# Kernel optimization log

Hardware: AMD Instinct MI355X
Metric: run time of the kernel (lower is better)

Reference implementation:

```python
import jax, jax.numpy as jnp
import numpy as np

V, H, B, S, J, T, NOP = 30000, 512, 16, 256, 10, 8, 4
NEG = -1e9


def setup_inputs() -> dict:
    key = jax.random.key(0)
    ks = jax.random.split(key, 10)
    return {
        "x": jax.random.randint(ks[0], (B, S), 0, V),
        "encoder_output": jax.random.normal(ks[1], (B, S, H), jnp.float32),
        "encoder_hidden": jax.random.normal(ks[2], (B, H), jnp.float32),
        "max_len": T,
        "emb_W": jax.random.normal(ks[3], (V, H), jnp.float32) * 0.02,
        "slot_emb": jax.random.normal(ks[4], (J, H), jnp.float32) * 0.1,
        "W_ih": jax.random.normal(ks[5], (3 * H, H), jnp.float32) * 0.02,
        "W_hh": jax.random.normal(ks[6], (3 * H, H), jnp.float32) * 0.02,
        "b_ih": jnp.zeros((3 * H,), jnp.float32),
        "b_hh": jnp.zeros((3 * H,), jnp.float32),
        "w_gen_W": jax.random.normal(ks[7], (1, 3 * H), jnp.float32) * 0.02,
        "w_gen_b": jnp.zeros((1,), jnp.float32),
        "action_W": jax.random.normal(ks[8], (NOP, H), jnp.float32) * 0.02,
        "action_b": jnp.zeros((NOP,), jnp.float32),
    }


def gru_step(xin, h, W_ih, W_hh, b_ih, b_hh):
    # xin, h: (J, B, H). PyTorch GRU gate order: r, z, n.
    gi = xin @ W_ih.T + b_ih
    gh = h @ W_hh.T + b_hh
    ir, iz, inn = jnp.split(gi, 3, axis=-1)
    hr, hz, hn = jnp.split(gh, 3, axis=-1)
    r = jax.nn.sigmoid(ir + hr)
    z = jax.nn.sigmoid(iz + hz)
    n = jnp.tanh(inn + r * hn)
    return (1.0 - z) * n + z * h


def reference(x, encoder_output, encoder_hidden, max_len, emb_W, slot_emb,
              W_ih, W_hh, b_ih, b_hh, w_gen_W, w_gen_b, action_W, action_b):
    nJ, nH = slot_emb.shape
    nB, nS = x.shape
    nV = emb_W.shape[0]
    mask = (x == 0)  # (B, S) pad mask
    xJ = jnp.broadcast_to(x[None], (nJ, nB, nS))
    jidx = jnp.arange(nJ)[:, None, None]
    bidx = jnp.arange(nB)[None, :, None]

    w0 = jnp.broadcast_to(slot_emb[:, None, :], (nJ, nB, nH))  # slot query per slot
    h0 = jnp.broadcast_to(encoder_hidden[None], (nJ, nB, nH))

    def step(carry, _):
        w, h = carry
        h = gru_step(w, h, W_ih, W_hh, b_ih, b_hh)
        # attention over encoder states
        attn_e = jnp.einsum('bsh,jbh->jbs', encoder_output, h)
        attn_e = jnp.where(mask[None], NEG, attn_e)
        attn_hist = jax.nn.softmax(attn_e, axis=-1)          # (J,B,S)
        context = jnp.einsum('jbs,bsh->jbh', attn_hist, encoder_output)
        # vocab distribution
        attn_vocab = jax.nn.softmax(h @ emb_W.T, axis=-1)    # (J,B,V)
        # pointer-generator mix
        gen_in = jnp.concatenate([w, h, context], axis=-1)   # (J,B,3H)
        p_gen = jax.nn.sigmoid(gen_in @ w_gen_W.T + w_gen_b) # (J,B,1)
        p_ctx = jnp.zeros((nJ, nB, nV), attn_vocab.dtype).at[jidx, bidx, xJ].add(attn_hist)
        p_final = p_gen * attn_vocab + (1.0 - p_gen) * p_ctx # (J,B,V)
        w_idx = jnp.argmax(p_final, axis=-1)                 # greedy next token
        w_next = emb_W[w_idx]                                # (J,B,H)
        return (w_next, h), (p_final, context)

    (_, _), (p_all, ctx_all) = jax.lax.scan(step, (w0, h0), None, length=max_len)
    # gate head uses context from first decode step (k == 0)
    gates = ctx_all[0] @ action_W.T + action_b               # (J,B,n_op)
    all_gate = jnp.transpose(gates, (1, 0, 2))               # (B,J,n_op)
    all_point = jnp.transpose(p_all, (2, 1, 0, 3))           # (B,J,T,V)
    return all_gate, all_point
```

## Files before the change

### kernel.cpp

```cpp
#include <hip/hip_runtime.h>
#include <math.h>

#define V 30000
#define H 512
#define NB 16
#define NS 256
#define NJ 10
#define NT 8
#define NOPS 4
#define NR 160
#define EV 30720
#define NEGV -1e9f
#define NTILES 1875
#define NVB 235

typedef __attribute__((ext_vector_type(8))) short short8;
typedef __attribute__((ext_vector_type(4))) short short4v;
typedef __attribute__((ext_vector_type(4))) float f32x4;

__device__ inline float bf2f(unsigned short s) {
    union { unsigned int u; float f; } c; c.u = ((unsigned int)s) << 16;
    return c.f;
}
__device__ inline unsigned short f2bf(float f) {
    union { float f; unsigned int u; } c; c.f = f;
    unsigned int u = c.u;
    u += 0x7fffu + ((u >> 16) & 1u);
    return (unsigned short)(u >> 16);
}
__device__ inline unsigned long long packkey(float f, int v) {
    union { float f; unsigned int u; } c; c.f = f;
    return ((unsigned long long)c.u << 32) | (unsigned int)(0x7FFFFFFF - v);
}

__global__ __launch_bounds__(256) void k_setup_pack(const float* __restrict__ emb,
                                                    unsigned short* __restrict__ emb_pk) {
    __shared__ unsigned short L[16 * 512];
    int nt = blockIdx.x;
    int t = threadIdx.x;
#pragma unroll
    for (int i = 0; i < 4; i++) {
        int o = i * 2048 + t * 8;
        int row = o >> 9, k = o & 511;
        const float4* src = (const float4*)(emb + (size_t)(nt * 16 + row) * 512 + k);
        float4 a = src[0], b = src[1];
        short8 v;
        v[0] = (short)f2bf(a.x); v[1] = (short)f2bf(a.y); v[2] = (short)f2bf(a.z); v[3] = (short)f2bf(a.w);
        v[4] = (short)f2bf(b.x); v[5] = (short)f2bf(b.y); v[6] = (short)f2bf(b.z); v[7] = (short)f2bf(b.w);
        *(short8*)(L + o) = v;
    }
    __syncthreads();
#pragma unroll
    for (int i = 0; i < 4; i++) {
        int idx = i * 256 + t;
        int ks = idx >> 6, l = idx & 63;
        int col15 = l & 15, quad = l >> 4;
        short8 v = *(const short8*)(L + col15 * 512 + ks * 32 + quad * 8);
        *(short8*)(emb_pk + ((size_t)(nt * 16 + ks) * 64 + l) * 8) = v;
    }
}

__global__ void k_setup_small(const float* __restrict__ Wih, const float* __restrict__ Whh,
    unsigned short* wih_hi, unsigned short* wih_lo, unsigned short* whh_hi, unsigned short* whh_lo,
    const float* __restrict__ slot, const float* __restrict__ ench,
    float* w_g, unsigned short* w_hi, unsigned short* w_lo,
    float* h_g, unsigned short* h_hi, unsigned short* h_lo, unsigned short* h_pk)
{
    int gid = blockIdx.x * 256 + threadIdx.x;
    if (gid < 786432) {
        float v1 = Wih[gid];
        unsigned short hi = f2bf(v1);
        wih_hi[gid] = hi; wih_lo[gid] = f2bf(v1 - bf2f(hi));
        float v2 = Whh[gid];
        hi = f2bf(v2);
        whh_hi[gid] = hi; whh_lo[gid] = f2bf(v2 - bf2f(hi));
    } else {
        int i = gid - 786432;
        if (i < NR * H) {
            int jb = i >> 9, d = i & 511;
            int j = jb >> 4, b = jb & 15;
            float wv = slot[j * H + d];
            w_g[i] = wv;
            unsigned short hi = f2bf(wv);
            w_hi[i] = hi; w_lo[i] = f2bf(wv - bf2f(hi));
            float hv = ench[b * H + d];
            h_g[i] = hv;
            hi = f2bf(hv);
            h_hi[i] = hi; h_lo[i] = f2bf(hv - bf2f(hi));
            int ks = d >> 5, quad = (d >> 3) & 3, e = d & 7;
            h_pk[(((jb >> 4) * 16 + ks) * 64 + quad * 16 + (jb & 15)) * 8 + e] = hi;
        }
    }
}

#define GRU_APAD 520
__global__ __launch_bounds__(256) void k_gru_gemm(
    const unsigned short* __restrict__ w_hi, const unsigned short* __restrict__ w_lo,
    const unsigned short* __restrict__ h_hi, const unsigned short* __restrict__ h_lo,
    const unsigned short* __restrict__ wih_hi, const unsigned short* __restrict__ wih_lo,
    const unsigned short* __restrict__ whh_hi, const unsigned short* __restrict__ whh_lo,
    float* __restrict__ gi, float* __restrict__ gh)
{
    __shared__ unsigned short Ah[16 * GRU_APAD];
    __shared__ unsigned short Al[16 * GRU_APAD];
    int nch = blockIdx.x, mt = blockIdx.y, z = blockIdx.z;
    const unsigned short* Asrc_hi = z ? h_hi : w_hi;
    const unsigned short* Asrc_lo = z ? h_lo : w_lo;
    const unsigned short* Bhi = z ? whh_hi : wih_hi;
    const unsigned short* Blo = z ? whh_lo : wih_lo;
    float* outp = z ? gh : gi;
    int t = threadIdx.x;
    for (int i = t; i < 2048; i += 256) {
        int matl = i >> 10;
        int row = (i >> 6) & 15;
        int seg = i & 63;
        const unsigned short* src = (matl ? Asrc_lo : Asrc_hi) + (mt * 16 + row) * 512 + seg * 8;
        unsigned short* dst = (matl ? Al : Ah) + row * GRU_APAD + seg * 8;
        *(short8*)dst = *(const short8*)src;
    }
    __syncthreads();
    int wv = t >> 6, lane = t & 63;
    int col15 = lane & 15, quad = lane >> 4;
    f32x4 acc0 = {0.f, 0.f, 0.f, 0.f}, acc1 = {0.f, 0.f, 0.f, 0.f};
    int c0 = nch * 128 + wv * 32 + col15;
    int c1 = c0 + 16;
    const unsigned short* bhp0 = Bhi + c0 * 512 + quad * 8;
    const unsigned short* bhp1 = Bhi + c1 * 512 + quad * 8;
    const unsigned short* blp0 = Blo + c0 * 512 + quad * 8;
    const unsigned short* blp1 = Blo + c1 * 512 + quad * 8;
    const unsigned short* ahp = Ah + col15 * GRU_APAD + quad * 8;
    const unsigned short* alp = Al + col15 * GRU_APAD + quad * 8;
#pragma unroll
    for (int ks = 0; ks < 16; ks++) {
        int ko = ks * 32;
        short8 bh0 = *(const short8*)(bhp0 + ko);
        short8 bh1 = *(const short8*)(bhp1 + ko);
        short8 bl0 = *(const short8*)(blp0 + ko);
        short8 bl1 = *(const short8*)(blp1 + ko);
        short8 ah = *(const short8*)(ahp + ko);
        short8 al = *(const short8*)(alp + ko);
        acc0 = __builtin_amdgcn_mfma_f32_16x16x32_bf16(ah, bh0, acc0, 0, 0, 0);
        acc1 = __builtin_amdgcn_mfma_f32_16x16x32_bf16(ah, bh1, acc1, 0, 0, 0);
        acc0 = __builtin_amdgcn_mfma_f32_16x16x32_bf16(ah, bl0, acc0, 0, 0, 0);
        acc1 = __builtin_amdgcn_mfma_f32_16x16x32_bf16(ah, bl1, acc1, 0, 0, 0);
        acc0 = __builtin_amdgcn_mfma_f32_16x16x32_bf16(al, bh0, acc0, 0, 0, 0);
        acc1 = __builtin_amdgcn_mfma_f32_16x16x32_bf16(al, bh1, acc1, 0, 0, 0);
    }
#pragma unroll
    for (int r = 0; r < 4; r++) {
        int row = mt * 16 + quad * 4 + r;
        outp[row * 1536 + c0] = acc0[r];
        outp[row * 1536 + c1] = acc1[r];
    }
}

__global__ __launch_bounds__(256) void k_attention(
    const float* __restrict__ gi, const float* __restrict__ gh,
    const float* __restrict__ b_ih, const float* __restrict__ b_hh,
    float* __restrict__ h_g, unsigned short* __restrict__ h_hi, unsigned short* __restrict__ h_lo,
    unsigned short* __restrict__ h_pk,
    const float* __restrict__ enc, const int* __restrict__ x,
    const float* __restrict__ w_g, const float* __restrict__ wgenW, const float* __restrict__ wgenb,
    float* __restrict__ attn_g, float* __restrict__ pgen_g,
    float* __restrict__ ctx0, int store_ctx)
{
    __shared__ float h_lds[512];
    __shared__ float sc[256];
    __shared__ float red[256];
    __shared__ float ctxp[4 * 512];
    int jb = blockIdx.x;
    int b = jb & 15;
    int t = threadIdx.x;
    int m_pk = jb >> 4, c_pk = jb & 15;
    for (int d = t; d < 512; d += 256) {
        int base = jb * 1536;
        float ir = gi[base + d]        + b_ih[d];
        float iz = gi[base + 512 + d]  + b_ih[512 + d];
        float in = gi[base + 1024 + d] + b_ih[1024 + d];
        float hr = gh[base + d]        + b_hh[d];
        float hz = gh[base + 512 + d]  + b_hh[512 + d];
        float hn = gh[base + 1024 + d] + b_hh[1024 + d];
        float hold = h_g[jb * 512 + d];
        float r = 1.f / (1.f + expf(-(ir + hr)));
        float z = 1.f / (1.f + expf(-(iz + hz)));
        float n = tanhf(in + r * hn);
        float hnew = (1.f - z) * n + z * hold;
        h_lds[d] = hnew;
        h_g[jb * 512 + d] = hnew;
        unsigned short hi = f2bf(hnew);
        h_hi[jb * 512 + d] = hi;
        h_lo[jb * 512 + d] = f2bf(hnew - bf2f(hi));
        int ks = d >> 5, quad = (d >> 3) & 3, e = d & 7;
        h_pk[((m_pk * 16 + ks) * 64 + quad * 16 + c_pk) * 8 + e] = hi;
    }
    __syncthreads();
    int wid = t >> 6, lane = t & 63;
    float hreg[8];
#pragma unroll
    for (int i = 0; i < 8; i++) hreg[i] = h_lds[lane * 8 + i];
    const float* encb = enc + (size_t)b * NS * H;
    for (int s = wid; s < NS; s += 4) {
        const float4* er = (const float4*)(encb + s * 512 + lane * 8);
        float4 e0 = er[0], e1 = er[1];
        float p = e0.x * hreg[0] + e0.y * hreg[1] + e0.z * hreg[2] + e0.w * hreg[3]
                + e1.x * hreg[4] + e1.y * hreg[5] + e1.z * hreg[6] + e1.w * hreg[7];
#pragma unroll
        for (int off = 32; off > 0; off >>= 1) p += __shfl_down(p, off);
        if (lane == 0) sc[s] = (x[b * NS + s] == 0) ? NEGV : p;
    }
    __syncthreads();
    red[t] = sc[t];
    __syncthreads();
    for (int sft = 128; sft > 0; sft >>= 1) { if (t < sft) red[t] = fmaxf(red[t], red[t + sft]); __syncthreads(); }
    float m = red[0];
    __syncthreads();
    float e = expf(sc[t] - m);
    red[t] = e;
    __syncthreads();
    for (int sft = 128; sft > 0; sft >>= 1) { if (t < sft) red[t] += red[t + sft]; __syncthreads(); }
    float inv = 1.f / red[0];
    float p_s = e * inv;
    sc[t] = p_s;
    attn_g[jb * NS + t] = p_s;
    __syncthreads();
    {
        float cp[8] = {0.f,0.f,0.f,0.f,0.f,0.f,0.f,0.f};
        const float* encw = encb + lane * 8;
        for (int s = wid * 64; s < wid * 64 + 64; s++) {
            float ps = sc[s];
            const float4* er = (const float4*)(encw + s * 512);
            float4 e0 = er[0], e1 = er[1];
            cp[0] += ps * e0.x; cp[1] += ps * e0.y; cp[2] += ps * e0.z; cp[3] += ps * e0.w;
            cp[4] += ps * e1.x; cp[5] += ps * e1.y; cp[6] += ps * e1.z; cp[7] += ps * e1.w;
        }
        float* cw = ctxp + wid * 512 + lane * 8;
#pragma unroll
        for (int i = 0; i < 8; i++) cw[i] = cp[i];
    }
    __syncthreads();
    int d0 = 2 * t, d1 = 2 * t + 1;
    float c0 = ctxp[d0] + ctxp[512 + d0] + ctxp[1024 + d0] + ctxp[1536 + d0];
    float c1 = ctxp[d1] + ctxp[512 + d1] + ctxp[1024 + d1] + ctxp[1536 + d1];
    if (store_ctx) ((float2*)ctx0)[jb * 256 + t] = make_float2(c0, c1);
    float pg = wgenW[d0] * w_g[jb * 512 + d0] + wgenW[d1] * w_g[jb * 512 + d1]
             + wgenW[512 + d0] * h_lds[d0] + wgenW[512 + d1] * h_lds[d1]
             + wgenW[1024 + d0] * c0 + wgenW[1024 + d1] * c1;
    __syncthreads();
    red[t] = pg;
    __syncthreads();
    for (int sft = 128; sft > 0; sft >>= 1) { if (t < sft) red[t] += red[t + sft]; __syncthreads(); }
    if (t == 0) pgen_g[jb] = 1.f / (1.f + expf(-(red[0] + wgenb[0])));
}

#define VPAD 136
__global__ __launch_bounds__(256) void k_vgemm(
    const unsigned short* __restrict__ h_pk, const unsigned short* __restrict__ emb_pk,
    unsigned short* __restrict__ E, float* __restrict__ rowsumP,
    unsigned long long* __restrict__ argpkP)
{
    __shared__ unsigned short A[160 * VPAD];
    int blk = blockIdx.x;
    int t = threadIdx.x;
    int wv = t >> 6, lane = t & 63, col15 = lane & 15, quad = lane >> 4;
    f32x4 acc[10][2];
#pragma unroll
    for (int m = 0; m < 10; m++) {
        acc[m][0] = (f32x4){0.f, 0.f, 0.f, 0.f};
        acc[m][1] = (f32x4){0.f, 0.f, 0.f, 0.f};
    }
    int nt0 = blk * 8 + wv * 2;
    int nt0c = min(nt0, NTILES - 1);
    int nt1c = min(nt0 + 1, NTILES - 1);
    for (int kc = 0; kc < 4; kc++) {
        __syncthreads();
#pragma unroll
        for (int i = 0; i < 10; i++) {
            int o = i * 2048 + t * 8;
            int m = o >> 11, rem = o & 2047;
            *(short8*)(A + m * 2048 + rem) =
                *(const short8*)(h_pk + (size_t)(m * 16 + kc * 4) * 512 + rem);
        }
        __syncthreads();
#pragma unroll
        for (int q = 0; q < 4; q++) {
            int ksg = kc * 4 + q;
            short8 b0 = *(const short8*)(emb_pk + ((size_t)(nt0c * 16 + ksg) * 64 + lane) * 8);
            short8 b1 = *(const short8*)(emb_pk + ((size_t)(nt1c * 16 + ksg) * 64 + lane) * 8);
#pragma unroll
            for (int m = 0; m < 10; m++) {
                short8 a = *(const short8*)(A + m * 2048 + q * 512 + lane * 8);
                acc[m][0] = __builtin_amdgcn_mfma_f32_16x16x32_bf16(a, b0, acc[m][0], 0, 0, 0);
                acc[m][1] = __builtin_amdgcn_mfma_f32_16x16x32_bf16(a, b1, acc[m][1], 0, 0, 0);
            }
        }
    }
    __syncthreads();
#pragma unroll
    for (int m = 0; m < 10; m++) {
#pragma unroll
        for (int tile = 0; tile < 2; tile++) {
            int cl = wv * 32 + tile * 16 + col15;
            int vv = blk * 128 + cl;
#pragma unroll
            for (int r = 0; r < 4; r++) {
                int row = m * 16 + quad * 4 + r;
                float ev = (vv < V) ? expf(acc[m][tile][r]) : 0.f;
                A[row * VPAD + cl] = f2bf(ev);
            }
        }
    }
    __syncthreads();
    if (t < 160) {
        float s = 0.f;
        unsigned long long key = 0ull;
#pragma unroll
        for (int seg = 0; seg < 16; seg++) {
            short8 ev = *(const short8*)(A + t * VPAD + seg * 8);
#pragma unroll
            for (int k = 0; k < 8; k++) {
                float f = bf2f((unsigned short)ev[k]);
                s += f;
                unsigned long long kk = packkey(f, blk * 128 + seg * 8 + k);
                key = (kk > key) ? kk : key;
            }
        }
        rowsumP[t * NVB + blk] = s;
        argpkP[t * NVB + blk] = key;
    }
    {
        int rsub = t >> 4, seg = t & 15;
        for (int it = 0; it < 10; it++) {
            int row = it * 16 + rsub;
            short8 ev = *(const short8*)(A + row * VPAD + seg * 8);
            *(short8*)(E + (size_t)row * EV + blk * 128 + seg * 8) = ev;
        }
    }
}

__global__ __launch_bounds__(256) void k_finalize(
    const unsigned short* __restrict__ E, const float* __restrict__ pgen_g,
    const float* __restrict__ rowsumP, const unsigned long long* __restrict__ argpkP,
    const float* __restrict__ attn_g, const int* __restrict__ x,
    const float* __restrict__ emb, float* __restrict__ out,
    float* __restrict__ w_g, unsigned short* __restrict__ w_hi, unsigned short* __restrict__ w_lo,
    const float* __restrict__ ctx0, const float* __restrict__ aW, const float* __restrict__ ab,
    int tstep)
{
    __shared__ float bvs[256];
    __shared__ int bis[256];
    __shared__ float red[256];
    __shared__ unsigned long long kred[256];
    int jb = blockIdx.x, t = threadIdx.x;
    int j = jb >> 4, b = jb & 15;
    red[t]  = (t < NVB) ? rowsumP[jb * NVB + t] : 0.f;
    kred[t] = (t < NVB) ? argpkP[jb * NVB + t] : 0ull;
    __syncthreads();
    for (int sft = 128; sft > 0; sft >>= 1) {
        if (t < sft) {
            red[t] += red[t + sft];
            if (kred[t + sft] > kred[t]) kred[t] = kred[t + sft];
        }
        __syncthreads();
    }
    float inv = 1.f / red[0];
    unsigned long long dkey = kred[0];
    float pgen = pgen_g[jb];
    float scale = pgen * inv;
    __syncthreads();
    const unsigned short* Er = E + (size_t)jb * EV;
    size_t outbase = (size_t)640 + ((size_t)(b * NJ + j) * NT + tstep) * V;
    float* op = out + outbase;
    for (int c = 0; c < 14; c++) {
        int vv = c * 2048 + t * 8;
        short8 e = *(const short8*)(Er + vv);
        float4 p0 = make_float4(bf2f((unsigned short)e[0]) * scale, bf2f((unsigned short)e[1]) * scale,
                                bf2f((unsigned short)e[2]) * scale, bf2f((unsigned short)e[3]) * scale);
        float4 p1 = make_float4(bf2f((unsigned short)e[4]) * scale, bf2f((unsigned short)e[5]) * scale,
                                bf2f((unsigned short)e[6]) * scale, bf2f((unsigned short)e[7]) * scale);
        *(float4*)(op + vv) = p0;
        *(float4*)(op + vv + 4) = p1;
    }
    if (t < 166) {
        int vv = 28672 + t * 8;
        short8 e = *(const short8*)(Er + vv);
        float4 p0 = make_float4(bf2f((unsigned short)e[0]) * scale, bf2f((unsigned short)e[1]) * scale,
                                bf2f((unsigned short)e[2]) * scale, bf2f((unsigned short)e[3]) * scale);
        float4 p1 = make_float4(bf2f((unsigned short)e[4]) * scale, bf2f((unsigned short)e[5]) * scale,
                                bf2f((unsigned short)e[6]) * scale, bf2f((unsigned short)e[7]) * scale);
        *(float4*)(op + vv) = p0;
        *(float4*)(op + vv + 4) = p1;
    }
    __syncthreads();
    float best; int besti;
    {
        int vv = x[b * NS + t];
        float a = (1.f - pgen) * attn_g[jb * NS + t];
        float old = atomicAdd(&op[vv], a);
        best = old + a;
        besti = vv;
    }
    bvs[t] = best; bis[t] = besti;
    __syncthreads();
    for (int sft = 128; sft > 0; sft >>= 1) {
        if (t < sft) {
            if (bvs[t + sft] > bvs[t] || (bvs[t + sft] == bvs[t] && bis[t + sft] < bis[t])) {
                bvs[t] = bvs[t + sft]; bis[t] = bis[t + sft];
            }
        }
        __syncthreads();
    }
    int widx;
    {
        union { unsigned int u; float f; } c; c.u = (unsigned int)(dkey >> 32);
        float db = c.f * scale;
        int di = 0x7FFFFFFF - (int)(dkey & 0xFFFFFFFFu);
        float sb = bvs[0]; int si = bis[0];
        widx = (sb > db || (sb == db && si < di)) ? si : di;
    }
    for (int d = t; d < 512; d += 256) {
        float val = emb[(size_t)widx * 512 + d];
        w_g[jb * 512 + d] = val;
        unsigned short hi = f2bf(val);
        w_hi[jb * 512 + d] = hi;
        w_lo[jb * 512 + d] = f2bf(val - bf2f(hi));
    }
    if (tstep == 0) {
        float part[4] = {0.f, 0.f, 0.f, 0.f};
        for (int d = t; d < 512; d += 256) {
            float c = ctx0[jb * 512 + d];
#pragma unroll
            for (int o = 0; o < 4; o++) part[o] += c * aW[o * 512 + d];
        }
        for (int o = 0; o < 4; o++) {
            __syncthreads();
            red[t] = part[o];
            __syncthreads();
            for (int sft = 128; sft > 0; sft >>= 1) { if (t < sft) red[t] += red[t + sft]; __syncthreads(); }
            if (t == 0) out[(b * NJ + j) * NOPS + o] = red[0] + ab[o];
        }
    }
}

extern "C" void kernel_launch(void* const* d_in, const int* in_sizes, int n_in,
                              void* d_out, int out_size, void* d_ws, size_t ws_size,
                              hipStream_t stream) {
    const int*   x     = (const int*)d_in[0];
    const float* enc   = (const float*)d_in[1];
    const float* ench  = (const float*)d_in[2];
    const float* embW  = (const float*)d_in[4];
    const float* slot  = (const float*)d_in[5];
    const float* Wih   = (const float*)d_in[6];
    const float* Whh   = (const float*)d_in[7];
    const float* bih   = (const float*)d_in[8];
    const float* bhh   = (const float*)d_in[9];
    const float* wgenW = (const float*)d_in[10];
    const float* wgenb = (const float*)d_in[11];
    const float* aW    = (const float*)d_in[12];
    const float* ab    = (const float*)d_in[13];
    float* out = (float*)d_out;

    char* ws = (char*)d_ws;
    size_t off = 0;
    auto carve = [&](size_t bytes) { char* p = ws + off; off += (bytes + 255) & ~(size_t)255; return p; };
    unsigned short* emb_pk = (unsigned short*)carve((size_t)V * H * 2);
    unsigned short* wih_hi = (unsigned short*)carve(786432 * 2);
    unsigned short* wih_lo = (unsigned short*)carve(786432 * 2);
    unsigned short* whh_hi = (unsigned short*)carve(786432 * 2);
    unsigned short* whh_lo = (unsigned short*)carve(786432 * 2);
    float* w_f32 = (float*)carve(NR * H * 4);
    float* h_f32 = (float*)carve(NR * H * 4);
    float* ctx0  = (float*)carve(NR * H * 4);
    unsigned short* w_hi = (unsigned short*)carve(NR * H * 2);
    unsigned short* w_lo = (unsigned short*)carve(NR * H * 2);
    unsigned short* h_hi = (unsigned short*)carve(NR * H * 2);
    unsigned short* h_lo = (unsigned short*)carve(NR * H * 2);
    unsigned short* h_pk = (unsigned short*)carve(NR * H * 2);
    float* gi   = (float*)carve(NR * 1536 * 4);
    float* gh   = (float*)carve(NR * 1536 * 4);
    float* attn = (float*)carve(NR * NS * 4);
    float* pgen = (float*)carve(NR * 4);
    float* rowsumP = (float*)carve((size_t)NR * NVB * 4);
    unsigned long long* argpkP = (unsigned long long*)carve((size_t)NR * NVB * 8);
    unsigned short* E = (unsigned short*)carve((size_t)NR * EV * 2);

    k_setup_pack<<<NTILES, 256, 0, stream>>>(embW, emb_pk);
    k_setup_small<<<3392, 256, 0, stream>>>(Wih, Whh, wih_hi, wih_lo, whh_hi, whh_lo,
                                            slot, ench, w_f32, w_hi, w_lo, h_f32, h_hi, h_lo, h_pk);
    for (int t = 0; t < NT; t++) {
        k_gru_gemm<<<dim3(12, 10, 2), 256, 0, stream>>>(w_hi, w_lo, h_hi, h_lo,
                                                        wih_hi, wih_lo, whh_hi, whh_lo, gi, gh);
        k_attention<<<NR, 256, 0, stream>>>(gi, gh, bih, bhh, h_f32, h_hi, h_lo, h_pk, enc, x,
                                            w_f32, wgenW, wgenb, attn, pgen, ctx0, t == 0 ? 1 : 0);
        k_vgemm<<<NVB, 256, 0, stream>>>(h_pk, emb_pk, E, rowsumP, argpkP);
        k_finalize<<<NR, 256, 0, stream>>>(E, pgen, rowsumP, argpkP, attn, x, embW, out,
                                           w_f32, w_hi, w_lo, ctx0, aW, ab, t);
    }
}
```

Before: 1.097 ms.

## Fuse per-step kernels into one persistent kernel with software grid barriers

The four kernels launched per decode step (GRU GEMM, attention, vocab GEMM, finalize), 32 launches in all, become one persistent 240-block kernel. It runs every step in a loop and separates phases with an atomic-counter grid barrier, with stages sharing one LDS buffer. This removes per-launch overhead and inter-kernel gaps, but lets idle blocks spin at barriers. It also relies on all 240 blocks being co-resident, which is not guaranteed without a cooperative launch.

```diff
diff --git a/kernel.cpp b/kernel.cpp
--- a/kernel.cpp
+++ b/kernel.cpp
@@ -13,9 +13,9 @@
 #define NEGV -1e9f
 #define NTILES 1875
 #define NVB 235
+#define NBLK 240
 
 typedef __attribute__((ext_vector_type(8))) short short8;
-typedef __attribute__((ext_vector_type(4))) short short4v;
 typedef __attribute__((ext_vector_type(4))) float f32x4;
 
 __device__ inline float bf2f(unsigned short s) {
@@ -31,6 +31,24 @@
 __device__ inline unsigned long long packkey(float f, int v) {
     union { float f; unsigned int u; } c; c.f = f;
     return ((unsigned long long)c.u << 32) | (unsigned int)(0x7FFFFFFF - v);
+}
+
+__device__ __forceinline__ void grid_sync(unsigned* cnt, unsigned* gen) {
+    __syncthreads();
+    if (threadIdx.x == 0) {
+        __threadfence();
+        unsigned g = __hip_atomic_load(gen, __ATOMIC_RELAXED, __HIP_MEMORY_SCOPE_AGENT);
+        unsigned a = __hip_atomic_fetch_add(cnt, 1u, __ATOMIC_ACQ_REL, __HIP_MEMORY_SCOPE_AGENT) + 1u;
+        if (a == (unsigned)NBLK) {
+            __hip_atomic_store(cnt, 0u, __ATOMIC_RELAXED, __HIP_MEMORY_SCOPE_AGENT);
+            __hip_atomic_store(gen, g + 1u, __ATOMIC_RELEASE, __HIP_MEMORY_SCOPE_AGENT);
+        } else {
+            while (__hip_atomic_load(gen, __ATOMIC_ACQUIRE, __HIP_MEMORY_SCOPE_AGENT) == g)
+                __builtin_amdgcn_s_sleep(1);
+        }
+        __threadfence();
+    }
+    __syncthreads();
 }
 
 __global__ __launch_bounds__(256) void k_setup_pack(const float* __restrict__ emb,
@@ -64,9 +82,11 @@
     unsigned short* wih_hi, unsigned short* wih_lo, unsigned short* whh_hi, unsigned short* whh_lo,
     const float* __restrict__ slot, const float* __restrict__ ench,
     float* w_g, unsigned short* w_hi, unsigned short* w_lo,
-    float* h_g, unsigned short* h_hi, unsigned short* h_lo, unsigned short* h_pk)
+    float* h_g, unsigned short* h_hi, unsigned short* h_lo, unsigned short* h_pk,
+    unsigned int* bar)
 {
     int gid = blockIdx.x * 256 + threadIdx.x;
+    if (gid == 0) { bar[0] = 0u; bar[1] = 0u; }
     if (gid < 786432) {
         float v1 = Wih[gid];
         unsigned short hi = f2bf(v1);
@@ -94,350 +114,346 @@
 }
 
 #define GRU_APAD 520
-__global__ __launch_bounds__(256) void k_gru_gemm(
-    const unsigned short* __restrict__ w_hi, const unsigned short* __restrict__ w_lo,
-    const unsigned short* __restrict__ h_hi, const unsigned short* __restrict__ h_lo,
+#define VPAD 136
+__global__ __launch_bounds__(256) void k_mega(
+    unsigned short* __restrict__ w_hi, unsigned short* __restrict__ w_lo,
+    unsigned short* __restrict__ h_hi, unsigned short* __restrict__ h_lo,
     const unsigned short* __restrict__ wih_hi, const unsigned short* __restrict__ wih_lo,
     const unsigned short* __restrict__ whh_hi, const unsigned short* __restrict__ whh_lo,
-    float* __restrict__ gi, float* __restrict__ gh)
+    float* __restrict__ gi, float* __restrict__ gh,
+    const float* __restrict__ b_ih, const float* __restrict__ b_hh,
+    float* __restrict__ h_g, unsigned short* __restrict__ h_pk,
+    const float* __restrict__ enc, const int* __restrict__ x,
+    float* __restrict__ w_g, const float* __restrict__ wgenW, const float* __restrict__ wgenb,
+    float* __restrict__ attn_g, float* __restrict__ pgen_g, float* __restrict__ ctx0,
+    const unsigned short* __restrict__ emb_pk, unsigned short* __restrict__ E,
+    float* __restrict__ rowsumP, unsigned long long* __restrict__ argpkP,
+    const float* __restrict__ emb, float* __restrict__ out,
+    const float* __restrict__ aW, const float* __restrict__ ab,
+    unsigned int* __restrict__ bar)
 {
-    __shared__ unsigned short Ah[16 * GRU_APAD];
-    __shared__ unsigned short Al[16 * GRU_APAD];
-    int nch = blockIdx.x, mt = blockIdx.y, z = blockIdx.z;
-    const unsigned short* Asrc_hi = z ? h_hi : w_hi;
-    const unsigned short* Asrc_lo = z ? h_lo : w_lo;
-    const unsigned short* Bhi = z ? whh_hi : wih_hi;
-    const unsigned short* Blo = z ? whh_lo : wih_lo;
-    float* outp = z ? gh : gi;
-    int t = threadIdx.x;
-    for (int i = t; i < 2048; i += 256) {
-        int matl = i >> 10;
-        int row = (i >> 6) & 15;
-        int seg = i & 63;
-        const unsigned short* src = (matl ? Asrc_lo : Asrc_hi) + (mt * 16 + row) * 512 + seg * 8;
-        unsigned short* dst = (matl ? Al : Ah) + row * GRU_APAD + seg * 8;
-        *(short8*)dst = *(const short8*)src;
-    }
-    __syncthreads();
+    __shared__ __attribute__((aligned(16))) unsigned long long smem_u64[5440];
+    char* smem = (char*)smem_u64;
+    unsigned int* cnt = bar;
+    unsigned int* gen = bar + 1;
+    int bid = blockIdx.x, t = threadIdx.x;
     int wv = t >> 6, lane = t & 63;
     int col15 = lane & 15, quad = lane >> 4;
-    f32x4 acc0 = {0.f, 0.f, 0.f, 0.f}, acc1 = {0.f, 0.f, 0.f, 0.f};
-    int c0 = nch * 128 + wv * 32 + col15;
-    int c1 = c0 + 16;
-    const unsigned short* bhp0 = Bhi + c0 * 512 + quad * 8;
-    const unsigned short* bhp1 = Bhi + c1 * 512 + quad * 8;
-    const unsigned short* blp0 = Blo + c0 * 512 + quad * 8;
-    const unsigned short* blp1 = Blo + c1 * 512 + quad * 8;
-    const unsigned short* ahp = Ah + col15 * GRU_APAD + quad * 8;
-    const unsigned short* alp = Al + col15 * GRU_APAD + quad * 8;
-#pragma unroll
-    for (int ks = 0; ks < 16; ks++) {
-        int ko = ks * 32;
-        short8 bh0 = *(const short8*)(bhp0 + ko);
-        short8 bh1 = *(const short8*)(bhp1 + ko);
-        short8 bl0 = *(const short8*)(blp0 + ko);
-        short8 bl1 = *(const short8*)(blp1 + ko);
-        short8 ah = *(const short8*)(ahp + ko);
-        short8 al = *(const short8*)(alp + ko);
-        acc0 = __builtin_amdgcn_mfma_f32_16x16x32_bf16(ah, bh0, acc0, 0, 0, 0);
-        acc1 = __builtin_amdgcn_mfma_f32_16x16x32_bf16(ah, bh1, acc1, 0, 0, 0);
-        acc0 = __builtin_amdgcn_mfma_f32_16x16x32_bf16(ah, bl0, acc0, 0, 0, 0);
-        acc1 = __builtin_amdgcn_mfma_f32_16x16x32_bf16(ah, bl1, acc1, 0, 0, 0);
-        acc0 = __builtin_amdgcn_mfma_f32_16x16x32_bf16(al, bh0, acc0, 0, 0, 0);
-        acc1 = __builtin_amdgcn_mfma_f32_16x16x32_bf16(al, bh1, acc1, 0, 0, 0);
-    }
-#pragma unroll
-    for (int r = 0; r < 4; r++) {
-        int row = mt * 16 + quad * 4 + r;
-        outp[row * 1536 + c0] = acc0[r];
-        outp[row * 1536 + c1] = acc1[r];
-    }
-}
-
-__global__ __launch_bounds__(256) void k_attention(
-    const float* __restrict__ gi, const float* __restrict__ gh,
-    const float* __restrict__ b_ih, const float* __restrict__ b_hh,
-    float* __restrict__ h_g, unsigned short* __restrict__ h_hi, unsigned short* __restrict__ h_lo,
-    unsigned short* __restrict__ h_pk,
-    const float* __restrict__ enc, const int* __restrict__ x,
-    const float* __restrict__ w_g, const float* __restrict__ wgenW, const float* __restrict__ wgenb,
-    float* __restrict__ attn_g, float* __restrict__ pgen_g,
-    float* __restrict__ ctx0, int store_ctx)
-{
-    __shared__ float h_lds[512];
-    __shared__ float sc[256];
-    __shared__ float red[256];
-    __shared__ float ctxp[4 * 512];
-    int jb = blockIdx.x;
-    int b = jb & 15;
-    int t = threadIdx.x;
-    int m_pk = jb >> 4, c_pk = jb & 15;
-    for (int d = t; d < 512; d += 256) {
-        int base = jb * 1536;
-        float ir = gi[base + d]        + b_ih[d];
-        float iz = gi[base + 512 + d]  + b_ih[512 + d];
-        float in = gi[base + 1024 + d] + b_ih[1024 + d];
-        float hr = gh[base + d]        + b_hh[d];
-        float hz = gh[base + 512 + d]  + b_hh[512 + d];
-        float hn = gh[base + 1024 + d] + b_hh[1024 + d];
-        float hold = h_g[jb * 512 + d];
-        float r = 1.f / (1.f + expf(-(ir + hr)));
-        float z = 1.f / (1.f + expf(-(iz + hz)));
-        float n = tanhf(in + r * hn);
-        float hnew = (1.f - z) * n + z * hold;
-        h_lds[d] = hnew;
-        h_g[jb * 512 + d] = hnew;
-        unsigned short hi = f2bf(hnew);
-        h_hi[jb * 512 + d] = hi;
-        h_lo[jb * 512 + d] = f2bf(hnew - bf2f(hi));
-        int ks = d >> 5, quad = (d >> 3) & 3, e = d & 7;
-        h_pk[((m_pk * 16 + ks) * 64 + quad * 16 + c_pk) * 8 + e] = hi;
-    }
-    __syncthreads();
-    int wid = t >> 6, lane = t & 63;
-    float hreg[8];
-#pragma unroll
-    for (int i = 0; i < 8; i++) hreg[i] = h_lds[lane * 8 + i];
-    const float* encb = enc + (size_t)b * NS * H;
-    for (int s = wid; s < NS; s += 4) {
-        const float4* er = (const float4*)(encb + s * 512 + lane * 8);
-        float4 e0 = er[0], e1 = er[1];
-        float p = e0.x * hreg[0] + e0.y * hreg[1] + e0.z * hreg[2] + e0.w * hreg[3]
-                + e1.x * hreg[4] + e1.y * hreg[5] + e1.z * hreg[6] + e1.w * hreg[7];
-#pragma unroll
-        for (int off = 32; off > 0; off >>= 1) p += __shfl_down(p, off);
-        if (lane == 0) sc[s] = (x[b * NS + s] == 0) ? NEGV : p;
-    }
-    __syncthreads();
-    red[t] = sc[t];
-    __syncthreads();
-    for (int sft = 128; sft > 0; sft >>= 1) { if (t < sft) red[t] = fmaxf(red[t], red[t + sft]); __syncthreads(); }
-    float m = red[0];
-    __syncthreads();
-    float e = expf(sc[t] - m);
-    red[t] = e;
-    __syncthreads();
-    for (int sft = 128; sft > 0; sft >>= 1) { if (t < sft) red[t] += red[t + sft]; __syncthreads(); }
-    float inv = 1.f / red[0];
-    float p_s = e * inv;
-    sc[t] = p_s;
-    attn_g[jb * NS + t] = p_s;
-    __syncthreads();
-    {
-        float cp[8] = {0.f,0.f,0.f,0.f,0.f,0.f,0.f,0.f};
-        const float* encw = encb + lane * 8;
-        for (int s = wid * 64; s < wid * 64 + 64; s++) {
-            float ps = sc[s];
-            const float4* er = (const float4*)(encw + s * 512);
-            float4 e0 = er[0], e1 = er[1];
-            cp[0] += ps * e0.x; cp[1] += ps * e0.y; cp[2] += ps * e0.z; cp[3] += ps * e0.w;
-            cp[4] += ps * e1.x; cp[5] += ps * e1.y; cp[6] += ps * e1.z; cp[7] += ps * e1.w;
+
+    for (int tstep = 0; tstep < NT; tstep++) {
+        {
+            unsigned short* Ah = (unsigned short*)smem;
+            unsigned short* Al = Ah + 16 * GRU_APAD;
+            int z = bid / 120, r2 = bid % 120;
+            int nch = r2 % 12, mt = r2 / 12;
+            const unsigned short* Asrc_hi = z ? h_hi : w_hi;
+            const unsigned short* Asrc_lo = z ? h_lo : w_lo;
+            const unsigned short* Bhi = z ? whh_hi : wih_hi;
+            const unsigned short* Blo = z ? whh_lo : wih_lo;
+            float* outp = z ? gh : gi;
+            for (int i = t; i < 2048; i += 256) {
+                int matl = i >> 10;
+                int row = (i >> 6) & 15;
+                int seg = i & 63;
+                const unsigned short* src = (matl ? Asrc_lo : Asrc_hi) + (mt * 16 + row) * 512 + seg * 8;
+                unsigned short* dst = (matl ? Al : Ah) + row * GRU_APAD + seg * 8;
+                *(short8*)dst = *(const short8*)src;
+            }
+            __syncthreads();
+            f32x4 acc0 = {0.f, 0.f, 0.f, 0.f}, acc1 = {0.f, 0.f, 0.f, 0.f};
+            int c0 = nch * 128 + wv * 32 + col15;
+            int c1 = c0 + 16;
+            const unsigned short* bhp0 = Bhi + c0 * 512 + quad * 8;
+            const unsigned short* bhp1 = Bhi + c1 * 512 + quad * 8;
+            const unsigned short* blp0 = Blo + c0 * 512 + quad * 8;
+            const unsigned short* blp1 = Blo + c1 * 512 + quad * 8;
+            const unsigned short* ahp = Ah + col15 * GRU_APAD + quad * 8;
+            const unsigned short* alp = Al + col15 * GRU_APAD + quad * 8;
+#pragma unroll
+            for (int ks = 0; ks < 16; ks++) {
+                int ko = ks * 32;
+                short8 bh0 = *(const short8*)(bhp0 + ko);
+                short8 bh1 = *(const short8*)(bhp1 + ko);
+                short8 bl0 = *(const short8*)(blp0 + ko);
+                short8 bl1 = *(const short8*)(blp1 + ko);
+                short8 ah = *(const short8*)(ahp + ko);
+                short8 al = *(const short8*)(alp + ko);
+                acc0 = __builtin_amdgcn_mfma_f32_16x16x32_bf16(ah, bh0, acc0, 0, 0, 0);
+                acc1 = __builtin_amdgcn_mfma_f32_16x16x32_bf16(ah, bh1, acc1, 0, 0, 0);
+                acc0 = __builtin_amdgcn_mfma_f32_16x16x32_bf16(ah, bl0, acc0, 0, 0, 0);
+                acc1 = __builtin_amdgcn_mfma_f32_16x16x32_bf16(ah, bl1, acc1, 0, 0, 0);
+                acc0 = __builtin_amdgcn_mfma_f32_16x16x32_bf16(al, bh0, acc0, 0, 0, 0);
+                acc1 = __builtin_amdgcn_mfma_f32_16x16x32_bf16(al, bh1, acc1, 0, 0, 0);
+            }
+#pragma unroll
+            for (int r = 0; r < 4; r++) {
+                int row = mt * 16 + quad * 4 + r;
+                outp[row * 1536 + c0] = acc0[r];
+                outp[row * 1536 + c1] = acc1[r];
+            }
         }
-        float* cw = ctxp + wid * 512 + lane * 8;
-#pragma unroll
-        for (int i = 0; i < 8; i++) cw[i] = cp[i];
-    }
-    __syncthreads();
-    int d0 = 2 * t, d1 = 2 * t + 1;
-    float c0 = ctxp[d0] + ctxp[512 + d0] + ctxp[1024 + d0] + ctxp[1536 + d0];
-    float c1 = ctxp[d1] + ctxp[512 + d1] + ctxp[1024 + d1] + ctxp[1536 + d1];
-    if (store_ctx) ((float2*)ctx0)[jb * 256 + t] = make_float2(c0, c1);
-    float pg = wgenW[d0] * w_g[jb * 512 + d0] + wgenW[d1] * w_g[jb * 512 + d1]
-             + wgenW[512 + d0] * h_lds[d0] + wgenW[512 + d1] * h_lds[d1]
-             + wgenW[1024 + d0] * c0 + wgenW[1024 + d1] * c1;
-    __syncthreads();
-    red[t] = pg;
-    __syncthreads();
-    for (int sft = 128; sft > 0; sft >>= 1) { if (t < sft) red[t] += red[t + sft]; __syncthreads(); }
-    if (t == 0) pgen_g[jb] = 1.f / (1.f + expf(-(red[0] + wgenb[0])));
-}
-
-#define VPAD 136
-__global__ __launch_bounds__(256) void k_vgemm(
-    const unsigned short* __restrict__ h_pk, const unsigned short* __restrict__ emb_pk,
-    unsigned short* __restrict__ E, float* __restrict__ rowsumP,
-    unsigned long long* __restrict__ argpkP)
-{
-    __shared__ unsigned short A[160 * VPAD];
-    int blk = blockIdx.x;
-    int t = threadIdx.x;
-    int wv = t >> 6, lane = t & 63, col15 = lane & 15, quad = lane >> 4;
-    f32x4 acc[10][2];
-#pragma unroll
-    for (int m = 0; m < 10; m++) {
-        acc[m][0] = (f32x4){0.f, 0.f, 0.f, 0.f};
-        acc[m][1] = (f32x4){0.f, 0.f, 0.f, 0.f};
-    }
-    int nt0 = blk * 8 + wv * 2;
-    int nt0c = min(nt0, NTILES - 1);
-    int nt1c = min(nt0 + 1, NTILES - 1);
-    for (int kc = 0; kc < 4; kc++) {
-        __syncthreads();
-#pragma unroll
-        for (int i = 0; i < 10; i++) {
-            int o = i * 2048 + t * 8;
-            int m = o >> 11, rem = o & 2047;
-            *(short8*)(A + m * 2048 + rem) =
-                *(const short8*)(h_pk + (size_t)(m * 16 + kc * 4) * 512 + rem);
+        grid_sync(cnt, gen);
+        if (bid < NR) {
+            float* h_lds = (float*)smem;
+            float* sc    = h_lds + 512;
+            float* red   = sc + 256;
+            float* ctxp  = red + 256;
+            int jb = bid;
+            int b = jb & 15;
+            int m_pk = jb >> 4, c_pk = jb & 15;
+            for (int d = t; d < 512; d += 256) {
+                int base = jb * 1536;
+                float ir = gi[base + d]        + b_ih[d];
+                float iz = gi[base + 512 + d]  + b_ih[512 + d];
+                float in = gi[base + 1024 + d] + b_ih[1024 + d];
+                float hr = gh[base + d]        + b_hh[d];
+                float hz = gh[base + 512 + d]  + b_hh[512 + d];
+                float hn = gh[base + 1024 + d] + b_hh[1024 + d];
+                float hold = h_g[jb * 512 + d];
+                float r = 1.f / (1.f + expf(-(ir + hr)));
+                float z = 1.f / (1.f + expf(-(iz + hz)));
+                float n = tanhf(in + r * hn);
+                float hnew = (1.f - z) * n + z * hold;
+                h_lds[d] = hnew;
+                h_g[jb * 512 + d] = hnew;
+                unsigned short hi = f2bf(hnew);
+                h_hi[jb * 512 + d] = hi;
+                h_lo[jb * 512 + d] = f2bf(hnew - bf2f(hi));
+                int ks = d >> 5, qd = (d >> 3) & 3, e = d & 7;
+                h_pk[((m_pk * 16 + ks) * 64 + qd * 16 + c_pk) * 8 + e] = hi;
+            }
+            __syncthreads();
+            float hreg[8];
+#pragma unroll
+            for (int i = 0; i < 8; i++) hreg[i] = h_lds[lane * 8 + i];
+            const float* encb = enc + (size_t)b * NS * H;
+            for (int s = wv; s < NS; s += 4) {
+                const float4* er = (const float4*)(encb + s * 512 + lane * 8);
+                float4 e0 = er[0], e1 = er[1];
+                float p = e0.x * hreg[0] + e0.y * hreg[1] + e0.z * hreg[2] + e0.w * hreg[3]
+                        + e1.x * hreg[4] + e1.y * hreg[5] + e1.z * hreg[6] + e1.w * hreg[7];
+#pragma unroll
+                for (int off = 32; off > 0; off >>= 1) p += __shfl_down(p, off);
+                if (lane == 0) sc[s] = (x[b * NS + s] == 0) ? NEGV : p;
+            }
+            __syncthreads();
+            red[t] = sc[t];
+            __syncthreads();
+            for (int sft = 128; sft > 0; sft >>= 1) { if (t < sft) red[t] = fmaxf(red[t], red[t + sft]); __syncthreads(); }
+            float m = red[0];
+            __syncthreads();
+            float e = expf(sc[t] - m);
+            red[t] = e;
+            __syncthreads();
+            for (int sft = 128; sft > 0; sft >>= 1) { if (t < sft) red[t] += red[t + sft]; __syncthreads(); }
+            float inv = 1.f / red[0];
+            float p_s = e * inv;
+            sc[t] = p_s;
+            attn_g[jb * NS + t] = p_s;
+            __syncthreads();
+            {
+                float cp[8] = {0.f,0.f,0.f,0.f,0.f,0.f,0.f,0.f};
+                const float* encw = encb + lane * 8;
+                for (int s = wv * 64; s < wv * 64 + 64; s++) {
+                    float ps = sc[s];
+                    const float4* er = (const float4*)(encw + s * 512);
+                    float4 e0 = er[0], e1 = er[1];
+                    cp[0] += ps * e0.x; cp[1] += ps * e0.y; cp[2] += ps * e0.z; cp[3] += ps * e0.w;
+                    cp[4] += ps * e1.x; cp[5] += ps * e1.y; cp[6] += ps * e1.z; cp[7] += ps * e1.w;
+                }
+                float* cw = ctxp + wv * 512 + lane * 8;
+#pragma unroll
+                for (int i = 0; i < 8; i++) cw[i] = cp[i];
+            }
+            __syncthreads();
+            int d0 = 2 * t, d1 = 2 * t + 1;
+            float c0 = ctxp[d0] + ctxp[512 + d0] + ctxp[1024 + d0] + ctxp[1536 + d0];
+            float c1 = ctxp[d1] + ctxp[512 + d1] + ctxp[1024 + d1] + ctxp[1536 + d1];
+            if (tstep == 0) ((float2*)ctx0)[jb * 256 + t] = make_float2(c0, c1);
+            float pg = wgenW[d0] * w_g[jb * 512 + d0] + wgenW[d1] * w_g[jb * 512 + d1]
+                     + wgenW[512 + d0] * h_lds[d0] + wgenW[512 + d1] * h_lds[d1]
+                     + wgenW[1024 + d0] * c0 + wgenW[1024 + d1] * c1;
+            __syncthreads();
+            red[t] = pg;
+            __syncthreads();
+            for (int sft = 128; sft > 0; sft >>= 1) { if (t < sft) red[t] += red[t + sft]; __syncthreads(); }
+            if (t == 0) pgen_g[jb] = 1.f / (1.f + expf(-(red[0] + wgenb[0])));
         }
-        __syncthreads();
-#pragma unroll
-        for (int q = 0; q < 4; q++) {
-            int ksg = kc * 4 + q;
-            short8 b0 = *(const short8*)(emb_pk + ((size_t)(nt0c * 16 + ksg) * 64 + lane) * 8);
-            short8 b1 = *(const short8*)(emb_pk + ((size_t)(nt1c * 16 + ksg) * 64 + lane) * 8);
+        grid_sync(cnt, gen);
+        if (bid < NVB) {
+            unsigned short* A = (unsigned short*)smem;
+            int blk = bid;
+            f32x4 acc[10][2];
 #pragma unroll
             for (int m = 0; m < 10; m++) {
-                short8 a = *(const short8*)(A + m * 2048 + q * 512 + lane * 8);
-                acc[m][0] = __builtin_amdgcn_mfma_f32_16x16x32_bf16(a, b0, acc[m][0], 0, 0, 0);
-                acc[m][1] = __builtin_amdgcn_mfma_f32_16x16x32_bf16(a, b1, acc[m][1], 0, 0, 0);
+                acc[m][0] = (f32x4){0.f, 0.f, 0.f, 0.f};
+                acc[m][1] = (f32x4){0.f, 0.f, 0.f, 0.f};
+            }
+            int nt0 = blk * 8 + wv * 2;
+            int nt0c = min(nt0, NTILES - 1);
+            int nt1c = min(nt0 + 1, NTILES - 1);
+            for (int kc = 0; kc < 4; kc++) {
+                __syncthreads();
+#pragma unroll
+                for (int i = 0; i < 10; i++) {
+                    int o = i * 2048 + t * 8;
+                    int m = o >> 11, rem = o & 2047;
+                    *(short8*)(A + m * 2048 + rem) =
+                        *(const short8*)(h_pk + (size_t)(m * 16 + kc * 4) * 512 + rem);
+                }
+                __syncthreads();
+#pragma unroll
+                for (int q = 0; q < 4; q++) {
+                    int ksg = kc * 4 + q;
+                    short8 b0 = *(const short8*)(emb_pk + ((size_t)(nt0c * 16 + ksg) * 64 + lane) * 8);
+                    short8 b1 = *(const short8*)(emb_pk + ((size_t)(nt1c * 16 + ksg) * 64 + lane) * 8);
+#pragma unroll
+                    for (int m = 0; m < 10; m++) {
+                        short8 a = *(const short8*)(A + m * 2048 + q * 512 + lane * 8);
+                        acc[m][0] = __builtin_amdgcn_mfma_f32_16x16x32_bf16(a, b0, acc[m][0], 0, 0, 0);
+                        acc[m][1] = __builtin_amdgcn_mfma_f32_16x16x32_bf16(a, b1, acc[m][1], 0, 0, 0);
+                    }
+                }
+            }
+            __syncthreads();
+#pragma unroll
+            for (int m = 0; m < 10; m++) {
+#pragma unroll
+                for (int tile = 0; tile < 2; tile++) {
+                    int cl = wv * 32 + tile * 16 + col15;
+                    int vvx = blk * 128 + cl;
+#pragma unroll
+                    for (int r = 0; r < 4; r++) {
+                        int row = m * 16 + quad * 4 + r;
+                        float ev = (vvx < V) ? expf(acc[m][tile][r]) : 0.f;
+                        A[row * VPAD + cl] = f2bf(ev);
+                    }
+                }
+            }
+            __syncthreads();
+            if (t < 160) {
+                float s = 0.f;
+                unsigned long long key = 0ull;
+#pragma unroll
+                for (int seg = 0; seg < 16; seg++) {
+                    short8 ev = *(const short8*)(A + t * VPAD + seg * 8);
+#pragma unroll
+                    for (int k = 0; k < 8; k++) {
+                        float f = bf2f((unsigned short)ev[k]);
+                        s += f;
+                        unsigned long long kk = packkey(f, blk * 128 + seg * 8 + k);
+                        key = (kk > key) ? kk : key;
+                    }
+                }
+                rowsumP[t * NVB + blk] = s;
+                argpkP[t * NVB + blk] = key;
+            }
+            {
+                int rsub = t >> 4, seg = t & 15;
+                for (int it = 0; it < 10; it++) {
+                    int row = it * 16 + rsub;
+                    short8 ev = *(const short8*)(A + row * VPAD + seg * 8);
+                    *(short8*)(E + (size_t)row * EV + blk * 128 + seg * 8) = ev;
+                }
             }
         }
-    }
-    __syncthreads();
-#pragma unroll
-    for (int m = 0; m < 10; m++) {
-#pragma unroll
-        for (int tile = 0; tile < 2; tile++) {
-            int cl = wv * 32 + tile * 16 + col15;
-            int vv = blk * 128 + cl;
-#pragma unroll
-            for (int r = 0; r < 4; r++) {
-                int row = m * 16 + quad * 4 + r;
-                float ev = (vv < V) ? expf(acc[m][tile][r]) : 0.f;
-                A[row * VPAD + cl] = f2bf(ev);
+        grid_sync(cnt, gen);
+        if (bid < NR) {
+            unsigned long long* kred = (unsigned long long*)smem;
+            float* bvs  = (float*)(smem + 2048);
+            int*   bis  = (int*)(smem + 3072);
+            float* redf = (float*)(smem + 4096);
+            int jb = bid;
+            int j = jb >> 4, b = jb & 15;
+            redf[t] = (t < NVB) ? rowsumP[jb * NVB + t] : 0.f;
+            kred[t] = (t < NVB) ? argpkP[jb * NVB + t] : 0ull;
+            __syncthreads();
+            for (int sft = 128; sft > 0; sft >>= 1) {
+                if (t < sft) {
+                    redf[t] += redf[t + sft];
+                    if (kred[t + sft] > kred[t]) kred[t] = kred[t + sft];
+                }
+                __syncthreads();
+            }
+            float inv = 1.f / redf[0];
+            unsigned long long dkey = kred[0];
+            float pgen = pgen_g[jb];
+            float scale = pgen * inv;
+            __syncthreads();
+            const unsigned short* Er = E + (size_t)jb * EV;
+            size_t outbase = (size_t)640 + ((size_t)(b * NJ + j) * NT + tstep) * V;
+            float* op = out + outbase;
+            for (int c = 0; c < 14; c++) {
+                int vvx = c * 2048 + t * 8;
+                short8 e = *(const short8*)(Er + vvx);
+                float4 p0 = make_float4(bf2f((unsigned short)e[0]) * scale, bf2f((unsigned short)e[1]) * scale,
+                                        bf2f((unsigned short)e[2]) * scale, bf2f((unsigned short)e[3]) * scale);
+                float4 p1 = make_float4(bf2f((unsigned short)e[4]) * scale, bf2f((unsigned short)e[5]) * scale,
+                                        bf2f((unsigned short)e[6]) * scale, bf2f((unsigned short)e[7]) * scale);
+                *(float4*)(op + vvx) = p0;
+                *(float4*)(op + vvx + 4) = p1;
+            }
+            if (t < 166) {
+                int vvx = 28672 + t * 8;
+                short8 e = *(const short8*)(Er + vvx);
+                float4 p0 = make_float4(bf2f((unsigned short)e[0]) * scale, bf2f((unsigned short)e[1]) * scale,
+                                        bf2f((unsigned short)e[2]) * scale, bf2f((unsigned short)e[3]) * scale);
+                float4 p1 = make_float4(bf2f((unsigned short)e[4]) * scale, bf2f((unsigned short)e[5]) * scale,
+                                        bf2f((unsigned short)e[6]) * scale, bf2f((unsigned short)e[7]) * scale);
+                *(float4*)(op + vvx) = p0;
+                *(float4*)(op + vvx + 4) = p1;
+            }
+            __syncthreads();
+            float best; int besti;
+            {
+                int vvx = x[b * NS + t];
+                float a = (1.f - pgen) * attn_g[jb * NS + t];
+                float old = atomicAdd(&op[vvx], a);
+                best = old + a;
+                besti = vvx;
+            }
+            bvs[t] = best; bis[t] = besti;
+            __syncthreads();
+            for (int sft = 128; sft > 0; sft >>= 1) {
+                if (t < sft) {
+                    if (bvs[t + sft] > bvs[t] || (bvs[t + sft] == bvs[t] && bis[t + sft] < bis[t])) {
+                        bvs[t] = bvs[t + sft]; bis[t] = bis[t + sft];
+                    }
+                }
+                __syncthreads();
+            }
+            int widx;
+            {
+                union { unsigned int u; float f; } c; c.u = (unsigned int)(dkey >> 32);
+                float db = c.f * scale;
+                int di = 0x7FFFFFFF - (int)(dkey & 0xFFFFFFFFu);
+                float sb = bvs[0]; int si = bis[0];
+                widx = (sb > db || (sb == db && si < di)) ? si : di;
+            }
+            for (int d = t; d < 512; d += 256) {
+                float val = emb[(size_t)widx * 512 + d];
+                w_g[jb * 512 + d] = val;
+                unsigned short hi = f2bf(val);
+                w_hi[jb * 512 + d] = hi;
+                w_lo[jb * 512 + d] = f2bf(val - bf2f(hi));
+            }
+            if (tstep == 0) {
+                float part[4] = {0.f, 0.f, 0.f, 0.f};
+                for (int d = t; d < 512; d += 256) {
+                    float c = ctx0[jb * 512 + d];
+#pragma unroll
+                    for (int o = 0; o < 4; o++) part[o] += c * aW[o * 512 + d];
+                }
+                for (int o = 0; o < 4; o++) {
+                    __syncthreads();
+                    redf[t] = part[o];
+                    __syncthreads();
+                    for (int sft = 128; sft > 0; sft >>= 1) { if (t < sft) redf[t] += redf[t + sft]; __syncthreads(); }
+                    if (t == 0) out[(b * NJ + j) * NOPS + o] = redf[0] + ab[o];
+                }
             }
         }
-    }
-    __syncthreads();
-    if (t < 160) {
-        float s = 0.f;
-        unsigned long long key = 0ull;
-#pragma unroll
-        for (int seg = 0; seg < 16; seg++) {
-            short8 ev = *(const short8*)(A + t * VPAD + seg * 8);
-#pragma unroll
-            for (int k = 0; k < 8; k++) {
-                float f = bf2f((unsigned short)ev[k]);
-                s += f;
-                unsigned long long kk = packkey(f, blk * 128 + seg * 8 + k);
-                key = (kk > key) ? kk : key;
-            }
-        }
-        rowsumP[t * NVB + blk] = s;
-        argpkP[t * NVB + blk] = key;
-    }
-    {
-        int rsub = t >> 4, seg = t & 15;
-        for (int it = 0; it < 10; it++) {
-            int row = it * 16 + rsub;
-            short8 ev = *(const short8*)(A + row * VPAD + seg * 8);
-            *(short8*)(E + (size_t)row * EV + blk * 128 + seg * 8) = ev;
-        }
-    }
-}
-
-__global__ __launch_bounds__(256) void k_finalize(
-    const unsigned short* __restrict__ E, const float* __restrict__ pgen_g,
-    const float* __restrict__ rowsumP, const unsigned long long* __restrict__ argpkP,
-    const float* __restrict__ attn_g, const int* __restrict__ x,
-    const float* __restrict__ emb, float* __restrict__ out,
-    float* __restrict__ w_g, unsigned short* __restrict__ w_hi, unsigned short* __restrict__ w_lo,
-    const float* __restrict__ ctx0, const float* __restrict__ aW, const float* __restrict__ ab,
-    int tstep)
-{
-    __shared__ float bvs[256];
-    __shared__ int bis[256];
-    __shared__ float red[256];
-    __shared__ unsigned long long kred[256];
-    int jb = blockIdx.x, t = threadIdx.x;
-    int j = jb >> 4, b = jb & 15;
-    red[t]  = (t < NVB) ? rowsumP[jb * NVB + t] : 0.f;
-    kred[t] = (t < NVB) ? argpkP[jb * NVB + t] : 0ull;
-    __syncthreads();
-    for (int sft = 128; sft > 0; sft >>= 1) {
-        if (t < sft) {
-            red[t] += red[t + sft];
-            if (kred[t + sft] > kred[t]) kred[t] = kred[t + sft];
-        }
-        __syncthreads();
-    }
-    float inv = 1.f / red[0];
-    unsigned long long dkey = kred[0];
-    float pgen = pgen_g[jb];
-    float scale = pgen * inv;
-    __syncthreads();
-    const unsigned short* Er = E + (size_t)jb * EV;
-    size_t outbase = (size_t)640 + ((size_t)(b * NJ + j) * NT + tstep) * V;
-    float* op = out + outbase;
-    for (int c = 0; c < 14; c++) {
-        int vv = c * 2048 + t * 8;
-        short8 e = *(const short8*)(Er + vv);
-        float4 p0 = make_float4(bf2f((unsigned short)e[0]) * scale, bf2f((unsigned short)e[1]) * scale,
-                                bf2f((unsigned short)e[2]) * scale, bf2f((unsigned short)e[3]) * scale);
-        float4 p1 = make_float4(bf2f((unsigned short)e[4]) * scale, bf2f((unsigned short)e[5]) * scale,
-                                bf2f((unsigned short)e[6]) * scale, bf2f((unsigned short)e[7]) * scale);
-        *(float4*)(op + vv) = p0;
-        *(float4*)(op + vv + 4) = p1;
-    }
-    if (t < 166) {
-        int vv = 28672 + t * 8;
-        short8 e = *(const short8*)(Er + vv);
-        float4 p0 = make_float4(bf2f((unsigned short)e[0]) * scale, bf2f((unsigned short)e[1]) * scale,
-                                bf2f((unsigned short)e[2]) * scale, bf2f((unsigned short)e[3]) * scale);
-        float4 p1 = make_float4(bf2f((unsigned short)e[4]) * scale, bf2f((unsigned short)e[5]) * scale,
-                                bf2f((unsigned short)e[6]) * scale, bf2f((unsigned short)e[7]) * scale);
-        *(float4*)(op + vv) = p0;
-        *(float4*)(op + vv + 4) = p1;
-    }
-    __syncthreads();
-    float best; int besti;
-    {
-        int vv = x[b * NS + t];
-        float a = (1.f - pgen) * attn_g[jb * NS + t];
-        float old = atomicAdd(&op[vv], a);
-        best = old + a;
-        besti = vv;
-    }
-    bvs[t] = best; bis[t] = besti;
-    __syncthreads();
-    for (int sft = 128; sft > 0; sft >>= 1) {
-        if (t < sft) {
-            if (bvs[t + sft] > bvs[t] || (bvs[t + sft] == bvs[t] && bis[t + sft] < bis[t])) {
-                bvs[t] = bvs[t + sft]; bis[t] = bis[t + sft];
-            }
-        }
-        __syncthreads();
-    }
-    int widx;
-    {
-        union { unsigned int u; float f; } c; c.u = (unsigned int)(dkey >> 32);
-        float db = c.f * scale;
-        int di = 0x7FFFFFFF - (int)(dkey & 0xFFFFFFFFu);
-        float sb = bvs[0]; int si = bis[0];
-        widx = (sb > db || (sb == db && si < di)) ? si : di;
-    }
-    for (int d = t; d < 512; d += 256) {
-        float val = emb[(size_t)widx * 512 + d];
-        w_g[jb * 512 + d] = val;
-        unsigned short hi = f2bf(val);
-        w_hi[jb * 512 + d] = hi;
-        w_lo[jb * 512 + d] = f2bf(val - bf2f(hi));
-    }
-    if (tstep == 0) {
-        float part[4] = {0.f, 0.f, 0.f, 0.f};
-        for (int d = t; d < 512; d += 256) {
-            float c = ctx0[jb * 512 + d];
-#pragma unroll
-            for (int o = 0; o < 4; o++) part[o] += c * aW[o * 512 + d];
-        }
-        for (int o = 0; o < 4; o++) {
-            __syncthreads();
-            red[t] = part[o];
-            __syncthreads();
-            for (int sft = 128; sft > 0; sft >>= 1) { if (t < sft) red[t] += red[t + sft]; __syncthreads(); }
-            if (t == 0) out[(b * NJ + j) * NOPS + o] = red[0] + ab[o];
-        }
+        if (tstep < NT - 1) grid_sync(cnt, gen);
     }
 }
 
@@ -481,18 +497,17 @@
     float* pgen = (float*)carve(NR * 4);
     float* rowsumP = (float*)carve((size_t)NR * NVB * 4);
     unsigned long long* argpkP = (unsigned long long*)carve((size_t)NR * NVB * 8);
+    unsigned int* bar = (unsigned int*)carve(256);
     unsigned short* E = (unsigned short*)carve((size_t)NR * EV * 2);
 
     k_setup_pack<<<NTILES, 256, 0, stream>>>(embW, emb_pk);
     k_setup_small<<<3392, 256, 0, stream>>>(Wih, Whh, wih_hi, wih_lo, whh_hi, whh_lo,
-                                            slot, ench, w_f32, w_hi, w_lo, h_f32, h_hi, h_lo, h_pk);
-    for (int t = 0; t < NT; t++) {
-        k_gru_gemm<<<dim3(12, 10, 2), 256, 0, stream>>>(w_hi, w_lo, h_hi, h_lo,
-                                                        wih_hi, wih_lo, whh_hi, whh_lo, gi, gh);
-        k_attention<<<NR, 256, 0, stream>>>(gi, gh, bih, bhh, h_f32, h_hi, h_lo, h_pk, enc, x,
-                                            w_f32, wgenW, wgenb, attn, pgen, ctx0, t == 0 ? 1 : 0);
-        k_vgemm<<<NVB, 256, 0, stream>>>(h_pk, emb_pk, E, rowsumP, argpkP);
-        k_finalize<<<NR, 256, 0, stream>>>(E, pgen, rowsumP, argpkP, attn, x, embW, out,
-                                           w_f32, w_hi, w_lo, ctx0, aW, ab, t);
-    }
-}
+                                            slot, ench, w_f32, w_hi, w_lo, h_f32, h_hi, h_lo, h_pk,
+                                            bar);
+    k_mega<<<NBLK, 256, 0, stream>>>(w_hi, w_lo, h_hi, h_lo,
+                                     wih_hi, wih_lo, whh_hi, whh_lo, gi, gh,
+                                     bih, bhh, h_f32, h_pk, enc, x,
+                                     w_f32, wgenW, wgenb, attn, pgen, ctx0,
+                                     emb_pk, E, rowsumP, argpkP,
+                                     embW, out, aW, ab, bar);
+}
```

Result: slower. 3.228 ms (+194.3%).
